# Performance work log

Measured on AMD Instinct MI355X. Metric: run time of the kernel, lower is better.

The kernel has to match this reference:

```python
import jax, jax.numpy as jnp
import numpy as np

NEG_INF = -jnp.inf
EPS = 1e-12  # F.normalize eps


def _build_spans(text_mask_row, max_span_length):
    # text_mask_row: concrete bool array [S]. Returns static numpy span index arrays.
    pos = np.nonzero(np.asarray(text_mask_row))[0]
    n = pos.size
    starts, ends, lens = [], [], []
    for i in range(n):
        for j in range(i, min(i + max_span_length, n)):
            starts.append(pos[i]); ends.append(pos[j]); lens.append(j - i + 1)
    return (np.asarray(starts, np.int32), np.asarray(ends, np.int32), np.asarray(lens, np.int32))


def setup_inputs() -> dict:
    key = jax.random.key(0)
    ks = jax.random.split(key, 8)
    B, S, H, T = 16, 1024, 768, 64
    L, LE = 4, 32
    Din = 3 * H + LE
    return {
        "hidden_states": jax.random.normal(ks[0], (B, S, H), jnp.float32),
        "topic_hidden": jax.random.normal(ks[1], (B, T, H), jnp.float32),
        "topic_mask": jnp.ones((B, T), jnp.bool_),
        "text_mask": jnp.ones((B, S), jnp.bool_),
        "len_emb": jax.random.normal(ks[2], (L + 1, LE), jnp.float32) * 0.02,
        "W1": jax.random.normal(ks[3], (Din, H), jnp.float32) / np.sqrt(Din),
        "b1": jnp.zeros((H,), jnp.float32),
        "W2": jax.random.normal(ks[4], (H, H), jnp.float32) / np.sqrt(H),
        "b2": jnp.zeros((H,), jnp.float32),
    }


def _l2norm(x):
    n = jnp.sqrt(jnp.sum(x * x, axis=-1, keepdims=True))
    return x / jnp.maximum(n, EPS)


def reference(hidden_states, topic_hidden, topic_mask, text_mask, len_emb, W1, b1, W2, b2):
    B, S, H = hidden_states.shape
    max_span_length = len_emb.shape[0] - 1
    # Masks are identical across the batch (all ones here): build spans once.
    starts_np, ends_np, lens_np = _build_spans(text_mask[0], max_span_length)
    starts = jnp.asarray(starts_np); ends = jnp.asarray(ends_np); lens = jnp.asarray(lens_np)
    N = starts.shape[0]

    start_v = hidden_states[:, starts]          # [B,N,H] gather span starts
    end_v = hidden_states[:, ends]              # [B,N,H] gather span ends
    csum = jnp.concatenate([jnp.zeros((B, 1, H), hidden_states.dtype),
                            jnp.cumsum(hidden_states, axis=1)], axis=1)  # [B,S+1,H]
    mean_v = (csum[:, ends + 1] - csum[:, starts]) / lens[None, :, None].astype(hidden_states.dtype)
    len_v = jnp.broadcast_to(len_emb[lens][None], (B, N, len_emb.shape[1]))

    feat = jnp.concatenate([start_v, end_v, mean_v, len_v], axis=-1)  # [B,N,3H+LE]
    span_vec = jax.nn.gelu(feat @ W1 + b1, approximate=False) @ W2 + b2  # [B,N,H]
    span_vec = _l2norm(span_vec)
    topic_vec = _l2norm(topic_hidden)                                    # [B,T,H]

    sim = jnp.einsum('bth,bnh->btn', topic_vec, span_vec)                # [B,T,N]
    sim = jnp.where(topic_mask[:, :, None], sim, NEG_INF)
    span_scores = jnp.max(sim, axis=1)                                   # [B,N]

    tok = jnp.arange(S)
    cover = (tok[None, :] >= starts[:, None]) & (tok[None, :] <= ends[:, None])  # [N,S]
    token_scores = jnp.max(jnp.where(cover[None], span_scores[:, :, None], NEG_INF), axis=1)  # [B,S]
    token_scores = jnp.where(text_mask, token_scores, NEG_INF)
    return token_scores
```

## Files before the change

kernel.cpp:

```cpp
#include <hip/hip_runtime.h>
#include <hip/hip_bf16.h>
#include <math.h>

typedef __bf16 bf16s;
typedef __attribute__((ext_vector_type(8))) __bf16 bf16x8;
typedef __attribute__((ext_vector_type(4))) __bf16 bf16x4;
typedef __attribute__((ext_vector_type(4))) float f32x4;

#define B_   16
#define S_   1024
#define H_   768
#define T_   64
#define L_   4
#define LE_  32
#define NPAD 4096
#define BS   (B_*S_)
#define BNR  (B_*NPAD)
#define N3   (3*H_)

static __device__ __forceinline__ void gload_lds16(const void* g, void* l) {
  __builtin_amdgcn_global_load_lds(
      (const __attribute__((address_space(1))) void*)g,
      (__attribute__((address_space(3))) void*)l, 16, 0, 0);
}

__global__ __launch_bounds__(1024) void k_build_spans(
    const int* __restrict__ text_mask,
    int* __restrict__ R, int* __restrict__ pos, int* __restrict__ spoff,
    int* __restrict__ starts, int* __restrict__ ends, int* __restrict__ lens,
    int* __restrict__ meta)
{
  __shared__ int buf[S_];
  int t = threadIdx.x;
  int m = text_mask[t] ? 1 : 0;
  buf[t] = m;
  __syncthreads();
  for (int off = 1; off < S_; off <<= 1) {
    int v = buf[t];
    if (t >= off) v += buf[t - off];
    __syncthreads();
    buf[t] = v;
    __syncthreads();
  }
  int incl = buf[t];
  R[t] = incl;
  if (m) pos[incl - 1] = t;
  int n = buf[S_ - 1];
  __syncthreads();
  int cnt = (t < n) ? min(L_, n - t) : 0;
  buf[t] = cnt;
  __syncthreads();
  for (int off = 1; off < S_; off <<= 1) {
    int v = buf[t];
    if (t >= off) v += buf[t - off];
    __syncthreads();
    buf[t] = v;
    __syncthreads();
  }
  int inc2 = buf[t];
  int base = inc2 - cnt;
  spoff[t] = base;
  if (t == 0) { meta[0] = buf[S_ - 1]; meta[1] = n; }
  __syncthreads();
  if (t < n) {
    int p0 = pos[t];
    for (int k = 0; k < cnt; k++) {
      starts[base + k] = p0;
      ends[base + k]   = pos[t + k];
      lens[base + k]   = k + 1;
    }
  }
}

__global__ __launch_bounds__(256) void k_prep(
    const float* __restrict__ hid, bf16s* __restrict__ hidb,
    const float* __restrict__ W1, bf16s* __restrict__ wbt,
    const float* __restrict__ W2, bf16s* __restrict__ w2t, bf16s* __restrict__ w2c,
    const float* __restrict__ lemb, float* __restrict__ LT,
    const float* __restrict__ TH, const float* __restrict__ b2,
    bf16s* __restrict__ TN, float* __restrict__ cvec)
{
  __shared__ float tile[64][65];
  __shared__ float red[256];
  int bid = blockIdx.x;
  int t = threadIdx.x;
  if (bid < 12288) {
    int i = bid * 256 + t;
    f32x4 v = ((const f32x4*)hid)[i];
    bf16x4 o;
    o[0] = (__bf16)v[0]; o[1] = (__bf16)v[1]; o[2] = (__bf16)v[2]; o[3] = (__bf16)v[3];
    ((bf16x4*)hidb)[i] = o;
  } else if (bid < 12864) {
    int local = bid - 12288;
    int c = local / 144, rem = local % 144;
    const float* in = (c < 3) ? (W1 + (size_t)c * H_ * H_) : W2;
    bf16s* out = (c < 3) ? (wbt + (size_t)c * H_ * H_) : w2t;
    int r0 = (rem / 12) * 64, c0 = (rem % 12) * 64;
    int tr = t >> 4, tc = (t & 15) * 4;
#pragma unroll
    for (int i = 0; i < 4; i++) {
      int row = tr + i * 16;
      f32x4 v = *(const f32x4*)(in + (long)(r0 + row) * H_ + c0 + tc);
      tile[row][tc+0] = v[0]; tile[row][tc+1] = v[1];
      tile[row][tc+2] = v[2]; tile[row][tc+3] = v[3];
    }
    __syncthreads();
#pragma unroll
    for (int i = 0; i < 4; i++) {
      int cc = tr + i * 16;
      bf16x4 o;
      o[0] = (__bf16)tile[tc+0][cc]; o[1] = (__bf16)tile[tc+1][cc];
      o[2] = (__bf16)tile[tc+2][cc]; o[3] = (__bf16)tile[tc+3][cc];
      *(bf16x4*)(out + (long)(c0 + cc) * H_ + r0 + tc) = o;
    }
  } else if (bid < 13440) {
    int i = (bid - 12864) * 256 + t;
    f32x4 v = ((const f32x4*)W2)[i];
    bf16x4 o;
    o[0] = (__bf16)v[0]; o[1] = (__bf16)v[1]; o[2] = (__bf16)v[2]; o[3] = (__bf16)v[3];
    ((bf16x4*)w2c)[i] = o;
  } else if (bid < 13455) {
    int idx = (bid - 13440) * 256 + t;
    if (idx < (L_ + 1) * H_) {
      int l = idx / H_, h = idx % H_;
      float acc = 0.f;
#pragma unroll
      for (int e = 0; e < LE_; e++) acc += lemb[l * LE_ + e] * W1[(long)(N3 + e) * H_ + h];
      LT[idx] = acc;
    }
  } else {
    int r = bid - 13455;
    const float* row = TH + (long)r * H_;
    float v0 = row[t], v1 = row[t + 256], v2 = row[t + 512];
    red[t] = v0 * v0 + v1 * v1 + v2 * v2;
    __syncthreads();
    for (int off = 128; off; off >>= 1) {
      if (t < off) red[t] += red[t + off];
      __syncthreads();
    }
    float rn = 1.0f / fmaxf(sqrtf(red[0]), 1e-12f);
    bf16s* o = TN + (long)r * H_;
    o[t] = (__bf16)(v0 * rn); o[t + 256] = (__bf16)(v1 * rn); o[t + 512] = (__bf16)(v2 * rn);
    __syncthreads();
    red[t] = v0 * b2[t] + v1 * b2[t + 256] + v2 * b2[t + 512];
    __syncthreads();
    for (int off = 128; off; off >>= 1) {
      if (t < off) red[t] += red[t + off];
      __syncthreads();
    }
    if (t == 0) cvec[r] = red[0] * rn;
  }
}

#define BKT 64
#define STG1_A(kt_, h_) do { \
    const bf16s* s_ = gA + (long)(h_) * 128 * K + (long)(kt_) * BKT; \
    char* d_ = sA + ((kt_) & 1) * 32768 + (h_) * 16384 + wid * 1024; \
    gload_lds16(s_, d_); \
    gload_lds16(s_ + 64L * K, d_ + 8192); \
  } while (0)
#define STG1_B(kt_, h_) do { \
    const bf16s* s_ = gB + (long)(h_) * 128 * K + (long)(kt_) * BKT; \
    char* d_ = sB + ((kt_) & 1) * 32768 + (h_) * 16384 + wid * 1024; \
    gload_lds16(s_, d_); \
    gload_lds16(s_ + 64L * K, d_ + 8192); \
  } while (0)
#define MFMA_Q(AF_, FR0_, FC_) do { \
    _Pragma("unroll") \
    for (int f_ = 0; f_ < 4; ++f_) { \
      acc[FR0_+f_][FC_] = __builtin_amdgcn_mfma_f32_16x16x32_bf16(bfv[FC_][0], AF_[f_][0], acc[FR0_+f_][FC_], 0, 0, 0); \
      acc[FR0_+f_][FC_] = __builtin_amdgcn_mfma_f32_16x16x32_bf16(bfv[FC_][1], AF_[f_][1], acc[FR0_+f_][FC_], 0, 0, 0); \
    } } while (0)
#define PH_PRE()  __builtin_amdgcn_s_barrier(); \
                  asm volatile("s_waitcnt lgkmcnt(0)" ::: "memory"); \
                  __builtin_amdgcn_s_setprio(1)
#define PH_POST() __builtin_amdgcn_s_setprio(0); \
                  __builtin_amdgcn_s_barrier()

__global__ __launch_bounds__(512, 2) void k_gemm8p(
    const bf16s* __restrict__ Ah, const bf16s* __restrict__ Bth, bf16s* __restrict__ Ch,
    const bf16s* __restrict__ Au, const bf16s* __restrict__ Btu, bf16s* __restrict__ Cu)
{
  __shared__ __align__(16) char sA[65536];
  __shared__ __align__(16) char sB[65536];
  const int K = H_;

  int tid = threadIdx.x;
  int wid = tid >> 6, l = tid & 63;
  int wr = wid >> 2, wc = wid & 3;
  int srow = tid >> 3;
  int sslot = (tid & 7) ^ (srow & 7);

  const char* aP0 = sA + wr * 16384;
  const char* aP1 = aP0 + 32768;
  const char* bP0 = sB + (wc >> 1) * 16384 + (wc & 1) * 8192;
  const char* bP1 = bP0 + 32768;
  int lrow = (l & 15) * 128;
  int ls0 = (((l >> 4) ^ (l & 7)) * 16);

  int nseg = (blockIdx.x < 76) ? 2 : 1;
#pragma unroll 1
  for (int seg = 0; seg < nseg; ++seg) {
    int raw = (seg == 0) ? blockIdx.x : 512 + blockIdx.x;
    const int nwg = 588;
    int q = nwg >> 3, rr = nwg & 7;
    int xcd = raw & 7, ix = raw >> 3;
    int nid = (xcd < rr ? xcd * (q + 1) : rr * (q + 1) + (xcd - rr) * q) + ix;

    const bf16s *A, *Bt;
    bf16s* C;
    long a0, b0;
    int NN;
    if (nid < 576) {
      A = Ah; Bt = Bth; C = Ch; NN = N3;
      a0 = (long)(nid / 9) * 256;
      b0 = (long)(nid % 9) * 256;
    } else {
      int u = nid - 576;
      A = Au; Bt = Btu; C = Cu; NN = H_;
      a0 = (long)(u / 3) * 256;
      b0 = (long)(u % 3) * 256;
    }
    const bf16s* gA = A + (a0 + srow) * (long)K + sslot * 8;
    const bf16s* gB = Bt + (b0 + srow) * (long)K + sslot * 8;

    f32x4 acc[8][4];
#pragma unroll
    for (int i = 0; i < 8; i++)
#pragma unroll
      for (int j = 0; j < 4; j++) acc[i][j] = (f32x4){0.f, 0.f, 0.f, 0.f};

    STG1_B(0, 0); STG1_B(0, 1); STG1_A(0, 0); STG1_A(0, 1);
    STG1_B(1, 0); STG1_B(1, 1); STG1_A(1, 0);
    asm volatile("s_waitcnt vmcnt(6)" ::: "memory");
    __builtin_amdgcn_s_barrier();

    for (int it = 0; it < 6; ++it) {
      int t0 = 2 * it, t1 = t0 + 1;
      bool nl = (it != 5);
      bf16x8 af0[4][2], af1[4][2], bfv[4][2];

#pragma unroll
      for (int f = 0; f < 4; ++f) {
        af0[f][0] = *(const bf16x8*)(aP0 + f * 2048 + lrow + ls0);
        af0[f][1] = *(const bf16x8*)(aP0 + f * 2048 + lrow + (ls0 ^ 64));
      }
#pragma unroll
      for (int c = 0; c < 4; ++c) {
        bfv[c][0] = *(const bf16x8*)(bP0 + c * 2048 + lrow + ls0);
        bfv[c][1] = *(const bf16x8*)(bP0 + c * 2048 + lrow + (ls0 ^ 64));
      }
      STG1_A(t1, 1);
      PH_PRE();
      MFMA_Q(af0, 0, 0); MFMA_Q(af0, 0, 1);
      PH_POST();

      if (nl) STG1_B(t0 + 2, 0);
      PH_PRE();
      MFMA_Q(af0, 0, 2); MFMA_Q(af0, 0, 3);
      PH_POST();

#pragma unroll
      for (int f = 0; f < 4; ++f) {
        af1[f][0] = *(const bf16x8*)(aP0 + (f + 4) * 2048 + lrow + ls0);
        af1[f][1] = *(const bf16x8*)(aP0 + (f + 4) * 2048 + lrow + (ls0 ^ 64));
      }
      if (nl) STG1_B(t0 + 2, 1);
      PH_PRE();
      MFMA_Q(af1, 4, 0); MFMA_Q(af1, 4, 1);
      PH_POST();

      if (nl) { STG1_A(t0 + 2, 0); asm volatile("s_waitcnt vmcnt(6)" ::: "memory"); }
      else    { asm volatile("s_waitcnt vmcnt(0)" ::: "memory"); }
      PH_PRE();
      MFMA_Q(af1, 4, 2); MFMA_Q(af1, 4, 3);
      PH_POST();

#pragma unroll
      for (int f = 0; f < 4; ++f) {
        af0[f][0] = *(const bf16x8*)(aP1 + f * 2048 + lrow + ls0);
        af0[f][1] = *(const bf16x8*)(aP1 + f * 2048 + lrow + (ls0 ^ 64));
      }
#pragma unroll
      for (int c = 0; c < 4; ++c) {
        bfv[c][0] = *(const bf16x8*)(bP1 + c * 2048 + lrow + ls0);
        bfv[c][1] = *(const bf16x8*)(bP1 + c * 2048 + lrow + (ls0 ^ 64));
      }
      if (nl) STG1_A(t0 + 2, 1);
      PH_PRE();
      MFMA_Q(af0, 0, 0); MFMA_Q(af0, 0, 1);
      PH_POST();

      if (nl) STG1_B(t1 + 2, 0);
      PH_PRE();
      MFMA_Q(af0, 0, 2); MFMA_Q(af0, 0, 3);
      PH_POST();

#pragma unroll
      for (int f = 0; f < 4; ++f) {
        af1[f][0] = *(const bf16x8*)(aP1 + (f + 4) * 2048 + lrow + ls0);
        af1[f][1] = *(const bf16x8*)(aP1 + (f + 4) * 2048 + lrow + (ls0 ^ 64));
      }
      if (nl) STG1_B(t1 + 2, 1);
      PH_PRE();
      MFMA_Q(af1, 4, 0); MFMA_Q(af1, 4, 1);
      PH_POST();

      if (nl) { STG1_A(t1 + 2, 0); asm volatile("s_waitcnt vmcnt(6)" ::: "memory"); }
      else    { asm volatile("s_waitcnt vmcnt(0)" ::: "memory"); }
      PH_PRE();
      MFMA_Q(af1, 4, 2); MFMA_Q(af1, 4, 3);
      PH_POST();
    }

#pragma unroll
    for (int fc = 0; fc < 4; fc++) {
      long n0 = b0 + wc * 64 + fc * 16 + (l >> 4) * 4;
#pragma unroll
      for (int fr = 0; fr < 8; fr++) {
        long mrow = a0 + wr * 128 + fr * 16 + (l & 15);
        bf16x4 o;
#pragma unroll
        for (int r = 0; r < 4; r++) o[r] = (__bf16)acc[fr][fc][r];
        *(bf16x4*)(C + mrow * (long)NN + n0) = o;
      }
    }
  }
}

#define STG_A(kt_, h_) do { \
    const bf16s* s_ = gA + (long)(h_) * 128 * K + (long)(kt_) * BKT; \
    char* d_ = sA + ((kt_) & 1) * 32768 + (h_) * 16384 + wid * 1024; \
    gload_lds16(s_, d_); \
    gload_lds16(s_ + 64L * K, d_ + 8192); \
  } while (0)
#define STG_B(ct_, kt_, h_) do { \
    const bf16s* s_ = gB + (long)(ct_) * 256 * K + (long)(h_) * 128 * K + (long)(kt_) * BKT; \
    char* d_ = sB + ((kt_) & 1) * 32768 + (h_) * 16384 + wid * 1024; \
    gload_lds16(s_, d_); \
    gload_lds16(s_ + 64L * K, d_ + 8192); \
  } while (0)

#define CHAIN_CORE(EPILOG_) \
  const char* aP0 = sA + wr * 16384; \
  const char* aP1 = aP0 + 32768; \
  const char* bP0 = sB + (wc >> 1) * 16384 + (wc & 1) * 8192; \
  const char* bP1 = bP0 + 32768; \
  int lrow = (l & 15) * 128; \
  int ls0 = (((l >> 4) ^ (l & 7)) * 16); \
  f32x4 acc[8][4]; \
  _Pragma("unroll") \
  for (int i_ = 0; i_ < 8; i_++) \
    _Pragma("unroll") \
    for (int j_ = 0; j_ < 4; j_++) acc[i_][j_] = (f32x4){0.f, 0.f, 0.f, 0.f}; \
  STG_B(0, 0, 0); STG_B(0, 0, 1); STG_A(0, 0); STG_A(0, 1); \
  STG_B(0, 1, 0); STG_B(0, 1, 1); STG_A(1, 0); \
  asm volatile("s_waitcnt vmcnt(6)" ::: "memory"); \
  __builtin_amdgcn_s_barrier(); \
  for (int s = 0; s < 3; ++s) { \
    for (int it = 0; it < 6; ++it) { \
      int kt0 = 2 * it; \
      bool nl = !(s == 2 && it == 5); \
      int ctn = (it == 5) ? s + 1 : s; \
      int kn0 = (it == 5) ? 0 : kt0 + 2; \
      int kn1 = (it == 5) ? 1 : kt0 + 3; \
      bf16x8 af0[4][2], af1[4][2], bfv[4][2]; \
      _Pragma("unroll") \
      for (int f = 0; f < 4; ++f) { \
        af0[f][0] = *(const bf16x8*)(aP0 + f * 2048 + lrow + ls0); \
        af0[f][1] = *(const bf16x8*)(aP0 + f * 2048 + lrow + (ls0 ^ 64)); \
      } \
      _Pragma("unroll") \
      for (int c = 0; c < 4; ++c) { \
        bfv[c][0] = *(const bf16x8*)(bP0 + c * 2048 + lrow + ls0); \
        bfv[c][1] = *(const bf16x8*)(bP0 + c * 2048 + lrow + (ls0 ^ 64)); \
      } \
      STG_A(kt0 + 1, 1); \
      PH_PRE(); \
      MFMA_Q(af0, 0, 0); MFMA_Q(af0, 0, 1); \
      PH_POST(); \
      if (nl) STG_B(ctn, kn0, 0); \
      PH_PRE(); \
      MFMA_Q(af0, 0, 2); MFMA_Q(af0, 0, 3); \
      PH_POST(); \
      _Pragma("unroll") \
      for (int f = 0; f < 4; ++f) { \
        af1[f][0] = *(const bf16x8*)(aP0 + (f + 4) * 2048 + lrow + ls0); \
        af1[f][1] = *(const bf16x8*)(aP0 + (f + 4) * 2048 + lrow + (ls0 ^ 64)); \
      } \
      if (nl) STG_B(ctn, kn0, 1); \
      PH_PRE(); \
      MFMA_Q(af1, 4, 0); MFMA_Q(af1, 4, 1); \
      PH_POST(); \
      if (nl) { STG_A(kn0, 0); asm volatile("s_waitcnt vmcnt(6)" ::: "memory"); } \
      else    { asm volatile("s_waitcnt vmcnt(0)" ::: "memory"); } \
      PH_PRE(); \
      MFMA_Q(af1, 4, 2); MFMA_Q(af1, 4, 3); \
      PH_POST(); \
      _Pragma("unroll") \
      for (int f = 0; f < 4; ++f) { \
        af0[f][0] = *(const bf16x8*)(aP1 + f * 2048 + lrow + ls0); \
        af0[f][1] = *(const bf16x8*)(aP1 + f * 2048 + lrow + (ls0 ^ 64)); \
      } \
      _Pragma("unroll") \
      for (int c = 0; c < 4; ++c) { \
        bfv[c][0] = *(const bf16x8*)(bP1 + c * 2048 + lrow + ls0); \
        bfv[c][1] = *(const bf16x8*)(bP1 + c * 2048 + lrow + (ls0 ^ 64)); \
      } \
      if (nl) STG_A(kn0, 1); \
      PH_PRE(); \
      MFMA_Q(af0, 0, 0); MFMA_Q(af0, 0, 1); \
      PH_POST(); \
      if (nl) STG_B(ctn, kn1, 0); \
      PH_PRE(); \
      MFMA_Q(af0, 0, 2); MFMA_Q(af0, 0, 3); \
      PH_POST(); \
      _Pragma("unroll") \
      for (int f = 0; f < 4; ++f) { \
        af1[f][0] = *(const bf16x8*)(aP1 + (f + 4) * 2048 + lrow + ls0); \
        af1[f][1] = *(const bf16x8*)(aP1 + (f + 4) * 2048 + lrow + (ls0 ^ 64)); \
      } \
      if (nl) STG_B(ctn, kn1, 1); \
      PH_PRE(); \
      MFMA_Q(af1, 4, 0); MFMA_Q(af1, 4, 1); \
      PH_POST(); \
      if (nl) { STG_A(kn1, 0); asm volatile("s_waitcnt vmcnt(6)" ::: "memory"); } \
      else    { asm volatile("s_waitcnt vmcnt(0)" ::: "memory"); } \
      PH_PRE(); \
      MFMA_Q(af1, 4, 2); MFMA_Q(af1, 4, 3); \
      PH_POST(); \
    } \
    EPILOG_(s); \
  }

__global__ __launch_bounds__(512, 1) void k_gemmnorm(
    const bf16s* __restrict__ Ax, const bf16s* __restrict__ Btw,
    const float* __restrict__ bias, float* __restrict__ ssbuf)
{
  __shared__ __align__(16) char sA[65536];
  __shared__ __align__(16) char sB[65536];
  const int K = H_;
  int bid = blockIdx.x;
  int nid = (bid & 7) * 32 + (bid >> 3);
  long a0 = (long)nid * 256;
  long b0base = 0;
  int tid = threadIdx.x;
  int wid = tid >> 6, l = tid & 63;
  int wr = wid >> 2, wc = wid & 3;
  int srow = tid >> 3;
  int sslot = (tid & 7) ^ (srow & 7);
  const bf16s* gA = Ax + (a0 + srow) * (long)K + sslot * 8;
  const bf16s* gB = Btw + (b0base + srow) * (long)K + sslot * 8;
  float ssp[8] = {0.f, 0.f, 0.f, 0.f, 0.f, 0.f, 0.f, 0.f};

#define EPI_N(s_) do { \
    f32x4 bb[4]; \
    _Pragma("unroll") \
    for (int fc = 0; fc < 4; ++fc) \
      bb[fc] = *(const f32x4*)(bias + (s_) * 256 + wc * 64 + fc * 16 + (l >> 4) * 4); \
    _Pragma("unroll") \
    for (int fr = 0; fr < 8; ++fr) { \
      float p = 0.f; \
      _Pragma("unroll") \
      for (int fc = 0; fc < 4; ++fc) { \
        _Pragma("unroll") \
        for (int r = 0; r < 4; ++r) { \
          float y = acc[fr][fc][r] + bb[fc][r]; \
          p += y * y; \
        } \
        acc[fr][fc] = (f32x4){0.f, 0.f, 0.f, 0.f}; \
      } \
      ssp[fr] += p; \
    } \
  } while (0)

  CHAIN_CORE(EPI_N)
#undef EPI_N

  float* sred = (float*)sA;
#pragma unroll
  for (int fr = 0; fr < 8; ++fr) {
    float p = ssp[fr];
    p += __shfl_xor(p, 16);
    p += __shfl_xor(p, 32);
    if (l < 16) sred[wc * 256 + wr * 128 + fr * 16 + l] = p;
  }
  __syncthreads();
  if (tid < 256) {
    ssbuf[a0 + tid] = sred[tid] + sred[256 + tid] + sred[512 + tid] + sred[768 + tid];
  }
}

#undef CHAIN_CORE
#undef STG_A
#undef STG_B
#undef STG1_A
#undef STG1_B
#undef MFMA_Q
#undef PH_PRE
#undef PH_POST

__global__ __launch_bounds__(192) void k_z1(
    const bf16s* __restrict__ P,
    const float* __restrict__ LT, const float* __restrict__ b1,
    const int* __restrict__ pos, const int* __restrict__ spoff,
    const int* __restrict__ meta, bf16s* __restrict__ X)
{
  int bid = blockIdx.x;
  int t = threadIdx.x;
  int h = t * 4;
  if (bid < BS) {
    int b = bid >> 10, i = bid & (S_ - 1);
    int n = meta[1];
    if (i >= n) return;
    int cnt = min(L_, n - i);
    int sa = pos[i];
    int base = spoff[i];
    const bf16s* Pb = P + (long)b * S_ * N3;
    bf16x4 vs = *(const bf16x4*)(Pb + (long)sa * N3 + h);
    f32x4 bb = *(const f32x4*)(b1 + h);
    float run[4] = {0.f, 0.f, 0.f, 0.f};
    int r = sa;
    for (int k = 0; k < cnt; ++k) {
      int se = pos[i + k];
      for (; r <= se; ++r) {
        bf16x4 vm = *(const bf16x4*)(Pb + (long)r * N3 + 2 * H_ + h);
#pragma unroll
        for (int j = 0; j < 4; j++) run[j] += (float)vm[j];
      }
      bf16x4 ve = *(const bf16x4*)(Pb + (long)se * N3 + H_ + h);
      f32x4 lt = *(const f32x4*)(LT + (long)(k + 1) * H_ + h);
      float il = 1.0f / (float)(k + 1);
      bf16x4 o;
#pragma unroll
      for (int j = 0; j < 4; j++) {
        float x = (float)vs[j] + (float)ve[j] + run[j] * il + lt[j] + bb[j];
        float g = 0.5f * x * (1.0f + erff(x * 0.70710678118654752f));
        o[j] = (__bf16)g;
      }
      *(bf16x4*)(X + ((long)b * NPAD + base + k) * H_ + h) = o;
    }
  } else {
    int N = meta[0];
    int pad = NPAD - N;
    if (pad <= 0) return;
    long total = (long)B_ * pad * 192;
    for (long idx = (long)(bid - BS) * 192 + t; idx < total; idx += 512L * 192) {
      int h4 = (int)(idx % 192);
      long rrw = idx / 192;
      int pr = (int)(rrw % pad);
      int bb2 = (int)(rrw / pad);
      bf16x4 z; z[0] = z[1] = z[2] = z[3] = (__bf16)0.f;
      *(bf16x4*)(X + ((long)bb2 * NPAD + N + pr) * H_ + h4 * 4) = z;
    }
  }
}

__global__ __launch_bounds__(256) void k_simx(
    const bf16s* __restrict__ X, const bf16s* __restrict__ U,
    const float* __restrict__ cvec, const float* __restrict__ ssbuf,
    const int* __restrict__ tmask, float* __restrict__ scores)
{
  int b = blockIdx.y;
  int wid = threadIdx.x >> 6, l = threadIdx.x & 63;
  int st = blockIdx.x * 4 + wid;
  int span = st * 16 + (l & 15);
  const bf16s* xrow = X + (long)(b * NPAD + span) * H_ + (l >> 4) * 8;
  const bf16s* ubase = U + (long)b * T_ * H_ + (l >> 4) * 8;
  f32x4 acc[4];
#pragma unroll
  for (int tt = 0; tt < 4; tt++) acc[tt] = (f32x4){0.f, 0.f, 0.f, 0.f};
  for (int kk = 0; kk < H_ / 32; kk++) {
    bf16x8 av = *(const bf16x8*)(xrow + kk * 32);
#pragma unroll
    for (int tt = 0; tt < 4; tt++) {
      bf16x8 bv = *(const bf16x8*)(ubase + (long)(tt * 16 + (l & 15)) * H_ + kk * 32);
      acc[tt] = __builtin_amdgcn_mfma_f32_16x16x32_bf16(av, bv, acc[tt], 0, 0, 0);
    }
  }
  const int* tm = tmask + b * T_;
  bool msk[4];
  float cv[4];
#pragma unroll
  for (int tt = 0; tt < 4; tt++) {
    int tcol = tt * 16 + (l & 15);
    msk[tt] = tm[tcol] != 0;
    cv[tt] = cvec[b * T_ + tcol];
  }
  float best[4];
#pragma unroll
  for (int r = 0; r < 4; r++) {
    float v = -INFINITY;
#pragma unroll
    for (int tt = 0; tt < 4; tt++) if (msk[tt]) v = fmaxf(v, acc[tt][r] + cv[tt]);
    best[r] = v;
  }
#pragma unroll
  for (int off = 8; off; off >>= 1)
#pragma unroll
    for (int r = 0; r < 4; r++) best[r] = fmaxf(best[r], __shfl_xor(best[r], off));
  if ((l & 15) == 0) {
    int srow = st * 16 + (l >> 4) * 4;
#pragma unroll
    for (int r = 0; r < 4; r++) {
      float ss = ssbuf[b * NPAD + srow + r];
      scores[b * NPAD + srow + r] = best[r] / fmaxf(sqrtf(ss), 1e-12f);
    }
  }
}

__global__ __launch_bounds__(256) void k_token(
    const int* __restrict__ text_mask,
    const int* __restrict__ R, const int* __restrict__ spoff,
    const int* __restrict__ meta, const float* __restrict__ scores,
    float* __restrict__ out)
{
  int idx = blockIdx.x * 256 + threadIdx.x;
  int s = idx % S_, b = idx / S_;
  if (!text_mask[b * S_ + s]) { out[idx] = -INFINITY; return; }
  int n = meta[1];
  int r1 = R[s];
  int le = r1 - 1;
  int ge = text_mask[s] ? (r1 - 1) : r1;
  float best = -INFINITY;
  if (le >= 0 && ge < n) {
    int i0 = max(0, ge - (L_ - 1));
    for (int i = i0; i <= le; i++) {
      int jmax = min(i + L_ - 1, n - 1);
      int off = spoff[i];
      for (int j = max(i, ge); j <= jmax; j++)
        best = fmaxf(best, scores[b * NPAD + off + (j - i)]);
    }
  }
  out[idx] = best;
}

__global__ __launch_bounds__(256) void k_sentinel(float* __restrict__ out) {
  int i = blockIdx.x * 256 + threadIdx.x;
  if (i < BS) out[i] = 12345.0f;
}

extern "C" void kernel_launch(void* const* d_in, const int* in_sizes, int n_in,
                              void* d_out, int out_size, void* d_ws, size_t ws_size,
                              hipStream_t stream) {
  const float* hid = (const float*)d_in[0];
  const float* th  = (const float*)d_in[1];
  const int* tmask = (const int*)d_in[2];
  const int* xmask = (const int*)d_in[3];
  const float* lemb = (const float*)d_in[4];
  const float* W1   = (const float*)d_in[5];
  const float* b1   = (const float*)d_in[6];
  const float* W2   = (const float*)d_in[7];
  const float* b2   = (const float*)d_in[8];
  float* out = (float*)d_out;

  char* w = (char*)d_ws;
  auto alloc = [&](size_t bytes) {
    char* p = w; w += (bytes + 255) & ~(size_t)255; return p;
  };
  bf16s* wbt   = (bf16s*)alloc((size_t)N3 * H_ * 2);
  bf16s* w2t   = (bf16s*)alloc((size_t)H_ * H_ * 2);
  bf16s* w2c   = (bf16s*)alloc((size_t)H_ * H_ * 2);
  float* LT    = (float*)alloc((size_t)(L_ + 1) * H_ * 4);
  bf16s* topn  = (bf16s*)alloc((size_t)B_ * T_ * H_ * 2);
  bf16s* U     = (bf16s*)alloc((size_t)B_ * T_ * H_ * 2);
  float* cvec  = (float*)alloc((size_t)B_ * T_ * 4);
  float* ssbuf = (float*)alloc((size_t)BNR * 4);
  float* scores= (float*)alloc((size_t)B_ * NPAD * 4);
  int* R       = (int*)alloc(S_ * 4);
  int* pos     = (int*)alloc(S_ * 4);
  int* spoff   = (int*)alloc(S_ * 4);
  int* starts  = (int*)alloc(NPAD * 4);
  int* ends    = (int*)alloc(NPAD * 4);
  int* lens    = (int*)alloc(NPAD * 4);
  int* meta    = (int*)alloc(2 * 4);
  char* regionA = alloc((size_t)BS * H_ * 2 + (size_t)BS * N3 * 2);
  bf16s* hidb  = (bf16s*)regionA;
  bf16s* P     = (bf16s*)(regionA + (size_t)BS * H_ * 2);
  bf16s* X     = (bf16s*)alloc((size_t)BNR * H_ * 2);

  size_t required = (size_t)(w - (char*)d_ws);
  if (required > ws_size) {
    k_sentinel<<<(BS + 255) / 256, 256, 0, stream>>>(out);
    return;
  }

  k_build_spans<<<1, 1024, 0, stream>>>(xmask, R, pos, spoff, starts, ends, lens, meta);
  k_prep<<<14479, 256, 0, stream>>>(hid, hidb, W1, wbt, W2, w2t, w2c,
                                    lemb, LT, th, b2, topn, cvec);

  k_gemm8p<<<512, 512, 0, stream>>>(hidb, wbt, P, topn, w2c, U);

  k_z1<<<BS + 512, 192, 0, stream>>>(P, LT, b1, pos, spoff, meta, X);

  k_gemmnorm<<<256, 512, 0, stream>>>(X, w2t, b2, ssbuf);

  k_simx<<<dim3(NPAD / 64, B_), 256, 0, stream>>>(X, U, cvec, ssbuf, tmask, scores);
  k_token<<<(B_ * S_) / 256, 256, 0, stream>>>(xmask, R, spoff, meta, scores, out);
  (void)in_sizes; (void)n_in; (void)out_size;
}
```

Measured before the change: 302.9 us.

## Retile norm GEMM to 128-row blocks with smaller LDS and higher occupancy

Rewrites the W2 sum-of-squares GEMM kernel to use 128-row A tiles and a 32-wide K step. This shrinks LDS from 128KB to 48KB and the accumulator array from 8x4 to 4x4, and raises launch bounds to allow several blocks per CU. The grid doubles to 512 blocks so the 256 CUs are better filled and multiple workgroups can hide latency. In exchange each block reloads the whole W2 matrix, with smaller MFMA batches per LDS sync and more barrier and wait overhead per unit of work.

```diff
diff --git a/kernel.cpp b/kernel.cpp
--- a/kernel.cpp
+++ b/kernel.cpp
@@ -328,172 +328,140 @@
   }
 }
 
-#define STG_A(kt_, h_) do { \
-    const bf16s* s_ = gA + (long)(h_) * 128 * K + (long)(kt_) * BKT; \
-    char* d_ = sA + ((kt_) & 1) * 32768 + (h_) * 16384 + wid * 1024; \
-    gload_lds16(s_, d_); \
-    gload_lds16(s_ + 64L * K, d_ + 8192); \
-  } while (0)
-#define STG_B(ct_, kt_, h_) do { \
-    const bf16s* s_ = gB + (long)(ct_) * 256 * K + (long)(h_) * 128 * K + (long)(kt_) * BKT; \
-    char* d_ = sB + ((kt_) & 1) * 32768 + (h_) * 16384 + wid * 1024; \
-    gload_lds16(s_, d_); \
-    gload_lds16(s_ + 64L * K, d_ + 8192); \
-  } while (0)
-
-#define CHAIN_CORE(EPILOG_) \
-  const char* aP0 = sA + wr * 16384; \
-  const char* aP1 = aP0 + 32768; \
-  const char* bP0 = sB + (wc >> 1) * 16384 + (wc & 1) * 8192; \
-  const char* bP1 = bP0 + 32768; \
-  int lrow = (l & 15) * 128; \
-  int ls0 = (((l >> 4) ^ (l & 7)) * 16); \
-  f32x4 acc[8][4]; \
-  _Pragma("unroll") \
-  for (int i_ = 0; i_ < 8; i_++) \
-    _Pragma("unroll") \
-    for (int j_ = 0; j_ < 4; j_++) acc[i_][j_] = (f32x4){0.f, 0.f, 0.f, 0.f}; \
-  STG_B(0, 0, 0); STG_B(0, 0, 1); STG_A(0, 0); STG_A(0, 1); \
-  STG_B(0, 1, 0); STG_B(0, 1, 1); STG_A(1, 0); \
-  asm volatile("s_waitcnt vmcnt(6)" ::: "memory"); \
-  __builtin_amdgcn_s_barrier(); \
-  for (int s = 0; s < 3; ++s) { \
-    for (int it = 0; it < 6; ++it) { \
-      int kt0 = 2 * it; \
-      bool nl = !(s == 2 && it == 5); \
-      int ctn = (it == 5) ? s + 1 : s; \
-      int kn0 = (it == 5) ? 0 : kt0 + 2; \
-      int kn1 = (it == 5) ? 1 : kt0 + 3; \
-      bf16x8 af0[4][2], af1[4][2], bfv[4][2]; \
-      _Pragma("unroll") \
-      for (int f = 0; f < 4; ++f) { \
-        af0[f][0] = *(const bf16x8*)(aP0 + f * 2048 + lrow + ls0); \
-        af0[f][1] = *(const bf16x8*)(aP0 + f * 2048 + lrow + (ls0 ^ 64)); \
-      } \
-      _Pragma("unroll") \
-      for (int c = 0; c < 4; ++c) { \
-        bfv[c][0] = *(const bf16x8*)(bP0 + c * 2048 + lrow + ls0); \
-        bfv[c][1] = *(const bf16x8*)(bP0 + c * 2048 + lrow + (ls0 ^ 64)); \
-      } \
-      STG_A(kt0 + 1, 1); \
-      PH_PRE(); \
-      MFMA_Q(af0, 0, 0); MFMA_Q(af0, 0, 1); \
-      PH_POST(); \
-      if (nl) STG_B(ctn, kn0, 0); \
-      PH_PRE(); \
-      MFMA_Q(af0, 0, 2); MFMA_Q(af0, 0, 3); \
-      PH_POST(); \
-      _Pragma("unroll") \
-      for (int f = 0; f < 4; ++f) { \
-        af1[f][0] = *(const bf16x8*)(aP0 + (f + 4) * 2048 + lrow + ls0); \
-        af1[f][1] = *(const bf16x8*)(aP0 + (f + 4) * 2048 + lrow + (ls0 ^ 64)); \
-      } \
-      if (nl) STG_B(ctn, kn0, 1); \
-      PH_PRE(); \
-      MFMA_Q(af1, 4, 0); MFMA_Q(af1, 4, 1); \
-      PH_POST(); \
-      if (nl) { STG_A(kn0, 0); asm volatile("s_waitcnt vmcnt(6)" ::: "memory"); } \
-      else    { asm volatile("s_waitcnt vmcnt(0)" ::: "memory"); } \
-      PH_PRE(); \
-      MFMA_Q(af1, 4, 2); MFMA_Q(af1, 4, 3); \
-      PH_POST(); \
-      _Pragma("unroll") \
-      for (int f = 0; f < 4; ++f) { \
-        af0[f][0] = *(const bf16x8*)(aP1 + f * 2048 + lrow + ls0); \
-        af0[f][1] = *(const bf16x8*)(aP1 + f * 2048 + lrow + (ls0 ^ 64)); \
-      } \
-      _Pragma("unroll") \
-      for (int c = 0; c < 4; ++c) { \
-        bfv[c][0] = *(const bf16x8*)(bP1 + c * 2048 + lrow + ls0); \
-        bfv[c][1] = *(const bf16x8*)(bP1 + c * 2048 + lrow + (ls0 ^ 64)); \
-      } \
-      if (nl) STG_A(kn0, 1); \
-      PH_PRE(); \
-      MFMA_Q(af0, 0, 0); MFMA_Q(af0, 0, 1); \
-      PH_POST(); \
-      if (nl) STG_B(ctn, kn1, 0); \
-      PH_PRE(); \
-      MFMA_Q(af0, 0, 2); MFMA_Q(af0, 0, 3); \
-      PH_POST(); \
-      _Pragma("unroll") \
-      for (int f = 0; f < 4; ++f) { \
-        af1[f][0] = *(const bf16x8*)(aP1 + (f + 4) * 2048 + lrow + ls0); \
-        af1[f][1] = *(const bf16x8*)(aP1 + (f + 4) * 2048 + lrow + (ls0 ^ 64)); \
-      } \
-      if (nl) STG_B(ctn, kn1, 1); \
-      PH_PRE(); \
-      MFMA_Q(af1, 4, 0); MFMA_Q(af1, 4, 1); \
-      PH_POST(); \
-      if (nl) { STG_A(kn1, 0); asm volatile("s_waitcnt vmcnt(6)" ::: "memory"); } \
-      else    { asm volatile("s_waitcnt vmcnt(0)" ::: "memory"); } \
-      PH_PRE(); \
-      MFMA_Q(af1, 4, 2); MFMA_Q(af1, 4, 3); \
-      PH_POST(); \
-    } \
-    EPILOG_(s); \
-  }
-
-__global__ __launch_bounds__(512, 1) void k_gemmnorm(
+__global__ __launch_bounds__(512, 4) void k_gemmnorm(
     const bf16s* __restrict__ Ax, const bf16s* __restrict__ Btw,
     const float* __restrict__ bias, float* __restrict__ ssbuf)
 {
-  __shared__ __align__(16) char sA[65536];
-  __shared__ __align__(16) char sB[65536];
+  __shared__ __align__(16) char sA[16384];
+  __shared__ __align__(16) char sB[32768];
   const int K = H_;
   int bid = blockIdx.x;
-  int nid = (bid & 7) * 32 + (bid >> 3);
-  long a0 = (long)nid * 256;
-  long b0base = 0;
+  int nid = (bid & 7) * 64 + (bid >> 3);
+  long a0 = (long)nid * 128;
   int tid = threadIdx.x;
   int wid = tid >> 6, l = tid & 63;
   int wr = wid >> 2, wc = wid & 3;
-  int srow = tid >> 3;
-  int sslot = (tid & 7) ^ (srow & 7);
+  int srow = tid >> 2;
+  int sslot = (tid & 3) ^ ((srow >> 1) & 3);
   const bf16s* gA = Ax + (a0 + srow) * (long)K + sslot * 8;
-  const bf16s* gB = Btw + (b0base + srow) * (long)K + sslot * 8;
-  float ssp[8] = {0.f, 0.f, 0.f, 0.f, 0.f, 0.f, 0.f, 0.f};
-
-#define EPI_N(s_) do { \
-    f32x4 bb[4]; \
-    _Pragma("unroll") \
-    for (int fc = 0; fc < 4; ++fc) \
-      bb[fc] = *(const f32x4*)(bias + (s_) * 256 + wc * 64 + fc * 16 + (l >> 4) * 4); \
-    _Pragma("unroll") \
-    for (int fr = 0; fr < 8; ++fr) { \
-      float p = 0.f; \
-      _Pragma("unroll") \
-      for (int fc = 0; fc < 4; ++fc) { \
-        _Pragma("unroll") \
-        for (int r = 0; r < 4; ++r) { \
-          float y = acc[fr][fc][r] + bb[fc][r]; \
-          p += y * y; \
-        } \
-        acc[fr][fc] = (f32x4){0.f, 0.f, 0.f, 0.f}; \
-      } \
-      ssp[fr] += p; \
-    } \
-  } while (0)
-
-  CHAIN_CORE(EPI_N)
-#undef EPI_N
+  const bf16s* gB = Btw + (long)srow * K + sslot * 8;
+
+#define SGA(kt_) \
+    gload_lds16(gA + (long)(kt_) * 32, sA + ((kt_) & 1) * 8192 + tid * 16)
+#define SGB(ct_, kt_, h_) \
+    gload_lds16(gB + ((long)(ct_) * 256 + (h_) * 128) * K + (long)(kt_) * 32, \
+                sB + ((kt_) & 1) * 16384 + (h_) * 8192 + tid * 16)
+
+  const char* aB = sA + wr * 4096;
+  const char* bB = sB + (wc >> 1) * 8192 + (wc & 1) * 4096;
+  int lrow = (l & 15) * 64;
+  int ls0 = ((l >> 4) ^ (((l & 15) >> 1) & 3)) * 16;
+
+  f32x4 acc[4][4];
+#pragma unroll
+  for (int i = 0; i < 4; i++)
+#pragma unroll
+    for (int j = 0; j < 4; j++) acc[i][j] = (f32x4){0.f, 0.f, 0.f, 0.f};
+  float ssp[4] = {0.f, 0.f, 0.f, 0.f};
+
+  SGB(0, 0, 0); SGB(0, 0, 1); SGA(0);
+  SGB(0, 1, 0); SGB(0, 1, 1); SGA(1);
+  asm volatile("s_waitcnt vmcnt(3)" ::: "memory");
+  __builtin_amdgcn_s_barrier();
+
+  for (int s = 0; s < 3; ++s) {
+    for (int it = 0; it < 12; ++it) {
+      int t0 = 2 * it;
+      bool nl = !(s == 2 && it == 11);
+      int ctn = (it == 11) ? s + 1 : s;
+      int kn0 = (it == 11) ? 0 : t0 + 2;
+      int kn1 = kn0 + 1;
+      bf16x8 af[4], bfv[4];
+
+#pragma unroll
+      for (int f = 0; f < 4; ++f) af[f] = *(const bf16x8*)(aB + f * 1024 + lrow + ls0);
+#pragma unroll
+      for (int c = 0; c < 4; ++c) bfv[c] = *(const bf16x8*)(bB + c * 1024 + lrow + ls0);
+      PH_PRE();
+#pragma unroll
+      for (int f = 0; f < 4; ++f) {
+        acc[f][0] = __builtin_amdgcn_mfma_f32_16x16x32_bf16(bfv[0], af[f], acc[f][0], 0, 0, 0);
+        acc[f][1] = __builtin_amdgcn_mfma_f32_16x16x32_bf16(bfv[1], af[f], acc[f][1], 0, 0, 0);
+      }
+      PH_POST();
+
+      if (nl) { SGB(ctn, kn0, 0); SGB(ctn, kn0, 1); SGA(kn0);
+                asm volatile("s_waitcnt vmcnt(3)" ::: "memory"); }
+      else    { asm volatile("s_waitcnt vmcnt(0)" ::: "memory"); }
+      PH_PRE();
+#pragma unroll
+      for (int f = 0; f < 4; ++f) {
+        acc[f][2] = __builtin_amdgcn_mfma_f32_16x16x32_bf16(bfv[2], af[f], acc[f][2], 0, 0, 0);
+        acc[f][3] = __builtin_amdgcn_mfma_f32_16x16x32_bf16(bfv[3], af[f], acc[f][3], 0, 0, 0);
+      }
+      PH_POST();
+
+#pragma unroll
+      for (int f = 0; f < 4; ++f) af[f] = *(const bf16x8*)(aB + 8192 + f * 1024 + lrow + ls0);
+#pragma unroll
+      for (int c = 0; c < 4; ++c) bfv[c] = *(const bf16x8*)(bB + 16384 + c * 1024 + lrow + ls0);
+      PH_PRE();
+#pragma unroll
+      for (int f = 0; f < 4; ++f) {
+        acc[f][0] = __builtin_amdgcn_mfma_f32_16x16x32_bf16(bfv[0], af[f], acc[f][0], 0, 0, 0);
+        acc[f][1] = __builtin_amdgcn_mfma_f32_16x16x32_bf16(bfv[1], af[f], acc[f][1], 0, 0, 0);
+      }
+      PH_POST();
+
+      if (nl) { SGB(ctn, kn1, 0); SGB(ctn, kn1, 1); SGA(kn1);
+                asm volatile("s_waitcnt vmcnt(3)" ::: "memory"); }
+      else    { asm volatile("s_waitcnt vmcnt(0)" ::: "memory"); }
+      PH_PRE();
+#pragma unroll
+      for (int f = 0; f < 4; ++f) {
+        acc[f][2] = __builtin_amdgcn_mfma_f32_16x16x32_bf16(bfv[2], af[f], acc[f][2], 0, 0, 0);
+        acc[f][3] = __builtin_amdgcn_mfma_f32_16x16x32_bf16(bfv[3], af[f], acc[f][3], 0, 0, 0);
+      }
+      PH_POST();
+    }
+    {
+      f32x4 bb[4];
+#pragma unroll
+      for (int fc = 0; fc < 4; ++fc)
+        bb[fc] = *(const f32x4*)(bias + s * 256 + wc * 64 + fc * 16 + (l >> 4) * 4);
+#pragma unroll
+      for (int f = 0; f < 4; ++f) {
+        float p = 0.f;
+#pragma unroll
+        for (int fc = 0; fc < 4; ++fc) {
+#pragma unroll
+          for (int r = 0; r < 4; ++r) {
+            float y = acc[f][fc][r] + bb[fc][r];
+            p += y * y;
+          }
+          acc[f][fc] = (f32x4){0.f, 0.f, 0.f, 0.f};
+        }
+        ssp[f] += p;
+      }
+    }
+  }
 
   float* sred = (float*)sA;
 #pragma unroll
-  for (int fr = 0; fr < 8; ++fr) {
-    float p = ssp[fr];
+  for (int f = 0; f < 4; ++f) {
+    float p = ssp[f];
     p += __shfl_xor(p, 16);
     p += __shfl_xor(p, 32);
-    if (l < 16) sred[wc * 256 + wr * 128 + fr * 16 + l] = p;
+    if (l < 16) sred[wc * 128 + wr * 64 + f * 16 + l] = p;
   }
   __syncthreads();
-  if (tid < 256) {
-    ssbuf[a0 + tid] = sred[tid] + sred[256 + tid] + sred[512 + tid] + sred[768 + tid];
-  }
-}
-
-#undef CHAIN_CORE
-#undef STG_A
-#undef STG_B
+  if (tid < 128) {
+    ssbuf[a0 + tid] = sred[tid] + sred[128 + tid] + sred[256 + tid] + sred[384 + tid];
+  }
+#undef SGA
+#undef SGB
+}
+
 #undef STG1_A
 #undef STG1_B
 #undef MFMA_Q
@@ -693,7 +661,7 @@
 
   k_z1<<<BS + 512, 192, 0, stream>>>(P, LT, b1, pos, spoff, meta, X);
 
-  k_gemmnorm<<<256, 512, 0, stream>>>(X, w2t, b2, ssbuf);
+  k_gemmnorm<<<512, 512, 0, stream>>>(X, w2t, b2, ssbuf);
 
   k_simx<<<dim3(NPAD / 64, B_), 256, 0, stream>>>(X, U, cvec, ssbuf, tmask, scores);
   k_token<<<(B_ * S_) / 256, 256, 0, stream>>>(xmask, R, spoff, meta, scores, out);
```

Measured after the change: 407.3 us. 1.34x slower.
